# Optimization experiments

Hardware: AMD Instinct MI355X
Metric: run time of the kernel (lower is better)

The kernel has to match this reference:

```python
import jax, jax.numpy as jnp
import numpy as np

KSIZE = 11
EPS = 1e-6

def _gauss_kernel(k=KSIZE, sigma=None):
    if sigma is None:
        sigma = k
    p = k // 2
    coords = np.arange(k) - p
    yy, xx = np.meshgrid(coords, coords, indexing='ij')
    g = np.exp(-(xx ** 2 + yy ** 2) / (2.0 * sigma ** 2))
    g = g / g.sum()
    return jnp.asarray(g, dtype=jnp.float32)

def setup_inputs() -> dict:
    key = jax.random.key(0)
    k1, k2 = jax.random.split(key)
    B, C, H, W = 16, 64, 256, 256
    x = jax.random.normal(k1, (B, C, H, W), dtype=jnp.float32)
    y = jax.random.normal(k2, (B, C, H, W), dtype=jnp.float32)
    gauss = _gauss_kernel()
    return {"x": x, "y": y, "gauss": gauss}

def reference(x, y, gauss):
    # Fused form: weighted local sums of x^2, y^2, x*y are SAME-padded
    # cross-correlations of the channel-summed products with the Gaussian.
    # This matches torch Unfold(padding=K//2) zero-padding semantics exactly.
    B, C, H, W = x.shape
    # channel-reduced local statistics inputs: [3, B, H, W]
    s = jnp.stack([
        jnp.sum(x * x, axis=1),
        jnp.sum(x * y, axis=1),
        jnp.sum(y * y, axis=1),
    ], axis=0)
    inp = s.reshape(3 * B, 1, H, W)              # NCHW
    ker = gauss[None, None, :, :]                # OIHW (symmetric -> corr==conv)
    out = jax.lax.conv_general_dilated(
        inp, ker, window_strides=(1, 1), padding='SAME',
        dimension_numbers=('NCHW', 'OIHW', 'NCHW'))
    xx, xy, yy = out.reshape(3, B, H, W)
    x_norm = jnp.sqrt(xx)
    y_norm = jnp.sqrt(yy)
    return xy / (x_norm * y_norm + EPS)
```

## Files before the change

kernel.cpp:

```cpp
#include <hip/hip_runtime.h>
#include <math.h>

constexpr int B = 16, C = 64, H = 256, W = 256;
constexpr int HW = H * W;
constexpr int BHW = B * HW;
constexpr int K = 11, P = 5;
#define EPS 1e-6f

__global__ __launch_bounds__(256) void k_reduce(
    const float* __restrict__ x, const float* __restrict__ y,
    float* __restrict__ s )
{
    const int GPI = HW / 4;
    int idx = blockIdx.x * 256 + threadIdx.x;
    int b = idx >> 14;
    int g = idx & (GPI - 1);

    const float4* x4 = (const float4*)x + (size_t)b * C * GPI + g;
    const float4* y4 = (const float4*)y + (size_t)b * C * GPI + g;

    float4 axx = make_float4(0.f, 0.f, 0.f, 0.f);
    float4 axy = axx, ayy = axx;

#pragma unroll 8
    for (int c = 0; c < C; ++c) {
        float4 xv = x4[c * GPI];
        float4 yv = y4[c * GPI];
        axx.x += xv.x * xv.x; axx.y += xv.y * xv.y;
        axx.z += xv.z * xv.z; axx.w += xv.w * xv.w;
        axy.x += xv.x * yv.x; axy.y += xv.y * yv.y;
        axy.z += xv.z * yv.z; axy.w += xv.w * yv.w;
        ayy.x += yv.x * yv.x; ayy.y += yv.y * yv.y;
        ayy.z += yv.z * yv.z; ayy.w += yv.w * yv.w;
    }

    float4* s4 = (float4*)s;
    int o = idx;
    s4[o]                 = axx;
    s4[(BHW / 4) + o]     = axy;
    s4[2 * (BHW / 4) + o] = ayy;
}


__global__ __launch_bounds__(256) void k_hblur(
    const float* __restrict__ s, const float* __restrict__ gauss,
    float* __restrict__ t )
{
    int idx = blockIdx.x * 256 + threadIdx.x;
    int w = idx & (W - 1);
    int rowbase = idx - w;

    float inv = 1.0f / sqrtf(gauss[5 * K + 5]);
    float wt[K];
#pragma unroll
    for (int j = 0; j < K; ++j) wt[j] = gauss[5 * K + j] * inv;

    float a0 = 0.f, a1 = 0.f, a2 = 0.f;
#pragma unroll
    for (int j = 0; j < K; ++j) {
        int ww = w + j - P;
        if (ww < 0 || ww >= W) continue;
        float wj = wt[j];
        a0 += wj * s[rowbase + ww];
        a1 += wj * s[BHW + rowbase + ww];
        a2 += wj * s[2 * BHW + rowbase + ww];
    }
    t[idx]           = a0;
    t[BHW + idx]     = a1;
    t[2 * BHW + idx] = a2;
}

__global__ __launch_bounds__(256) void k_vblur_combine(
    const float* __restrict__ t, const float* __restrict__ gauss,
    float* __restrict__ out )
{
    int idx = blockIdx.x * 256 + threadIdx.x;
    int hw = idx & (HW - 1);
    int h = hw >> 8;

    float inv = 1.0f / sqrtf(gauss[5 * K + 5]);
    float wt[K];
#pragma unroll
    for (int i = 0; i < K; ++i) wt[i] = gauss[i * K + 5] * inv;

    float axx = 0.f, axy = 0.f, ayy = 0.f;
#pragma unroll
    for (int i = 0; i < K; ++i) {
        int hh = h + i - P;
        if (hh < 0 || hh >= H) continue;
        float wi = wt[i];
        int off = idx + (i - P) * W;
        axx += wi * t[off];
        axy += wi * t[BHW + off];
        ayy += wi * t[2 * BHW + off];
    }
    out[idx] = axy / (sqrtf(axx) * sqrtf(ayy) + EPS);
}

extern "C" void kernel_launch(void* const* d_in, const int* in_sizes, int n_in,
                              void* d_out, int out_size, void* d_ws, size_t ws_size,
                              hipStream_t stream) {
    const float* x     = (const float*)d_in[0];
    const float* y     = (const float*)d_in[1];
    const float* gauss = (const float*)d_in[2];
    float* out = (float*)d_out;

    float* s = (float*)d_ws;
    float* t = s + 3 * BHW;

    k_reduce<<<B * (HW / 4) / 256, 256, 0, stream>>>(x, y, s);
    k_hblur<<<BHW / 256, 256, 0, stream>>>(s, gauss, t);
    k_vblur_combine<<<BHW / 256, 256, 0, stream>>>(t, gauss, out);
}
```

Baseline: 545.0 us.

## Fuse horizontal and vertical blur into one LDS-banded kernel, batch reduce loads

Merges the separate horizontal-blur and vertical-blur/combine kernels into one kernel. Each block processes an 8-row band per image: it horizontally blurs 18 rows into shared memory, then vertically blurs and combines. This removes the intermediate t buffer round-trip through global memory and one launch, at the cost of recomputing halo rows (18 of every 8) and per-row __syncthreads with low occupancy from about 57KB of LDS per block. The reduce kernel also now issues eight float4 loads per input before accumulating, to get more memory requests in flight.

```diff
diff --git a/kernel.cpp b/kernel.cpp
--- a/kernel.cpp
+++ b/kernel.cpp
@@ -22,16 +22,25 @@
     float4 axx = make_float4(0.f, 0.f, 0.f, 0.f);
     float4 axy = axx, ayy = axx;
 
-#pragma unroll 8
-    for (int c = 0; c < C; ++c) {
-        float4 xv = x4[c * GPI];
-        float4 yv = y4[c * GPI];
-        axx.x += xv.x * xv.x; axx.y += xv.y * xv.y;
-        axx.z += xv.z * xv.z; axx.w += xv.w * xv.w;
-        axy.x += xv.x * yv.x; axy.y += xv.y * yv.y;
-        axy.z += xv.z * yv.z; axy.w += xv.w * yv.w;
-        ayy.x += yv.x * yv.x; ayy.y += yv.y * yv.y;
-        ayy.z += yv.z * yv.z; ayy.w += yv.w * yv.w;
+    float4 xv[8], yv[8];
+#pragma unroll 1
+    for (int c = 0; c < C; c += 8) {
+#pragma unroll
+        for (int u = 0; u < 8; ++u) {
+            xv[u] = x4[u * GPI];
+            yv[u] = y4[u * GPI];
+        }
+        x4 += 8 * GPI;
+        y4 += 8 * GPI;
+#pragma unroll
+        for (int u = 0; u < 8; ++u) {
+            axx.x += xv[u].x * xv[u].x; axx.y += xv[u].y * xv[u].y;
+            axx.z += xv[u].z * xv[u].z; axx.w += xv[u].w * xv[u].w;
+            axy.x += xv[u].x * yv[u].x; axy.y += xv[u].y * yv[u].y;
+            axy.z += xv[u].z * yv[u].z; axy.w += xv[u].w * yv[u].w;
+            ayy.x += yv[u].x * yv[u].x; ayy.y += yv[u].y * yv[u].y;
+            ayy.z += yv[u].z * yv[u].z; ayy.w += yv[u].w * yv[u].w;
+        }
     }
 
     float4* s4 = (float4*)s;
@@ -41,60 +50,67 @@
     s4[2 * (BHW / 4) + o] = ayy;
 }
 
+constexpr int R = 8;
+constexpr int BAND = R + 2 * P;
 
-__global__ __launch_bounds__(256) void k_hblur(
+__global__ __launch_bounds__(256) void k_blur_combine(
     const float* __restrict__ s, const float* __restrict__ gauss,
-    float* __restrict__ t )
-{
-    int idx = blockIdx.x * 256 + threadIdx.x;
-    int w = idx & (W - 1);
-    int rowbase = idx - w;
-
-    float inv = 1.0f / sqrtf(gauss[5 * K + 5]);
-    float wt[K];
-#pragma unroll
-    for (int j = 0; j < K; ++j) wt[j] = gauss[5 * K + j] * inv;
-
-    float a0 = 0.f, a1 = 0.f, a2 = 0.f;
-#pragma unroll
-    for (int j = 0; j < K; ++j) {
-        int ww = w + j - P;
-        if (ww < 0 || ww >= W) continue;
-        float wj = wt[j];
-        a0 += wj * s[rowbase + ww];
-        a1 += wj * s[BHW + rowbase + ww];
-        a2 += wj * s[2 * BHW + rowbase + ww];
-    }
-    t[idx]           = a0;
-    t[BHW + idx]     = a1;
-    t[2 * BHW + idx] = a2;
-}
-
-__global__ __launch_bounds__(256) void k_vblur_combine(
-    const float* __restrict__ t, const float* __restrict__ gauss,
     float* __restrict__ out )
 {
-    int idx = blockIdx.x * 256 + threadIdx.x;
-    int hw = idx & (HW - 1);
-    int h = hw >> 8;
+    __shared__ float hb[BAND * 3 * W];
+    __shared__ float raw[3 * W];
 
-    float inv = 1.0f / sqrtf(gauss[5 * K + 5]);
-    float wt[K];
+    const int t = threadIdx.x;
+    const int blk = blockIdx.x;
+    const int b = blk >> 5;
+    const int band = blk & 31;
+    const int r0 = band * R;
+
+    const float inv = 1.0f / sqrtf(gauss[5 * K + 5]);
+    float wrow[K], wcol[K];
 #pragma unroll
-    for (int i = 0; i < K; ++i) wt[i] = gauss[i * K + 5] * inv;
+    for (int j = 0; j < K; ++j) wrow[j] = gauss[5 * K + j] * inv;
+#pragma unroll
+    for (int i = 0; i < K; ++i) wcol[i] = gauss[i * K + 5] * inv;
 
-    float axx = 0.f, axy = 0.f, ayy = 0.f;
+    for (int r = 0; r < BAND; ++r) {
+        int gr = r0 - P + r;
+        bool v = (gr >= 0) && (gr < H);
+        int rowoff = b * HW + gr * W + t;
+        raw[0 * W + t] = v ? s[rowoff] : 0.f;
+        raw[1 * W + t] = v ? s[BHW + rowoff] : 0.f;
+        raw[2 * W + t] = v ? s[2 * BHW + rowoff] : 0.f;
+        __syncthreads();
+        float a0 = 0.f, a1 = 0.f, a2 = 0.f;
 #pragma unroll
-    for (int i = 0; i < K; ++i) {
-        int hh = h + i - P;
-        if (hh < 0 || hh >= H) continue;
-        float wi = wt[i];
-        int off = idx + (i - P) * W;
-        axx += wi * t[off];
-        axy += wi * t[BHW + off];
-        ayy += wi * t[2 * BHW + off];
+        for (int j = 0; j < K; ++j) {
+            int c = t + j - P;
+            if (c >= 0 && c < W) {
+                float wj = wrow[j];
+                a0 += wj * raw[0 * W + c];
+                a1 += wj * raw[1 * W + c];
+                a2 += wj * raw[2 * W + c];
+            }
+        }
+        hb[(r * 3 + 0) * W + t] = a0;
+        hb[(r * 3 + 1) * W + t] = a1;
+        hb[(r * 3 + 2) * W + t] = a2;
+        __syncthreads();
     }
-    out[idx] = axy / (sqrtf(axx) * sqrtf(ayy) + EPS);
+
+#pragma unroll
+    for (int rr = 0; rr < R; ++rr) {
+        float axx = 0.f, axy = 0.f, ayy = 0.f;
+#pragma unroll
+        for (int i = 0; i < K; ++i) {
+            float wi = wcol[i];
+            int rb = ((rr + i) * 3) * W + t;
+            axx += wi * hb[rb];
+            axy += wi * hb[rb + W];
+            ayy += wi * hb[rb + 2 * W];
+        }
+        out[b * HW + (r0 + rr) * W + t] = axy / (sqrtf(axx) * sqrtf(ayy) + EPS);
+    }
 }
 
 extern "C" void kernel_launch(void* const* d_in, const int* in_sizes, int n_in,
@@ -106,9 +122,7 @@
     float* out = (float*)d_out;
 
     float* s = (float*)d_ws;
-    float* t = s + 3 * BHW;
 
     k_reduce<<<B * (HW / 4) / 256, 256, 0, stream>>>(x, y, s);
-    k_hblur<<<BHW / 256, 256, 0, stream>>>(s, gauss, t);
-    k_vblur_combine<<<BHW / 256, 256, 0, stream>>>(t, gauss, out);
+    k_blur_combine<<<B * (H / R), 256, 0, stream>>>(s, gauss, out);
 }
```

After: 546.5 us. About the same (+0.3%).
